# Optimization experiments

Hardware: AMD Instinct MI355X
Metric: run time of the kernel (lower is better)

The kernel has to match this reference:

```python
import jax, jax.numpy as jnp
import numpy as np

jax.config.update("jax_enable_x64", True)  # original torch code runs in float64; minors underflow fp32

D = 96   # Nsites
N = 48   # Nparticles


def setup_inputs() -> dict:
    key = jax.random.key(0)
    # Orthonormal single-particle orbitals (columns), as the module assumes (P^T P = I)
    A = jax.random.normal(key, (D, D), dtype=jnp.float64)
    Q, _ = jnp.linalg.qr(A)
    P = Q[:, :N]  # [D, N]
    # A valid ordered particle configuration: strictly increasing, occ_positions[k] <= D-N+k
    occ_positions = jnp.arange(N, dtype=jnp.int32) * (D // N)  # stride-2 filling
    return {"P": P, "occ_positions": occ_positions}


def _cond_probs(P, occ_positions):
    """Conditional probabilities probs[k, x] of placing the k-th (ordered) particle at
    site x given particles 0..k-1 at occ_positions[0..k-1].

    Math identical to SlaterDetSampler_ordered.get_cond_prob (naive_update=True):
      G = I - P P^T
      probs[k,x] = -det(M_x[0:x+1,0:x+1]) / det(M[0:xmin,0:xmin])
    where M = G - diag(occupancy of particles < k) and M_x additionally sets n_x = 1.
    Since Ksites is always the contiguous range 0..x, all determinants are LEADING
    principal minors; and because only the (x,x) diagonal entry changes by -1 (last index
    of the block), det(M_x block) = d_{x+1} - d_x with d_j the leading j-minor of M.
    """
    Dd, Nn = P.shape
    dt = P.dtype
    eye = jnp.eye(Dd, dtype=dt)
    G = eye - P @ P.T                                             # [D, D]

    onehots = jax.nn.one_hot(occ_positions, Dd, dtype=dt)         # [N, D]
    n_before = jnp.cumsum(onehots, axis=0) - onehots              # occupancy of particles < k
    A = G[None] - n_before[:, :, None] * eye                      # [N, D, D]: G - diag(n_<k)

    # All leading principal minors via batched det of masked matrices:
    # M_j = A on the [0:j,0:j] block, identity elsewhere  =>  det(M_j) = leading j-minor
    ii = jnp.arange(Dd)
    jj = jnp.arange(1, Dd + 1)
    blk = (ii[None, :, None] < jj[:, None, None]) & (ii[None, None, :] < jj[:, None, None])  # [D,D,D]
    Ms = jnp.where(blk[None], A[:, None], eye)                    # [N, D, D, D]
    d = jnp.linalg.det(Ms.reshape(Nn * Dd, Dd, Dd)).reshape(Nn, Dd)
    d_full = jnp.concatenate([jnp.ones((Nn, 1), dt), d], axis=1)  # d_full[k, j] = j-th leading minor

    k = jnp.arange(Nn)
    xmin = jnp.where(k == 0, 0, occ_positions[jnp.maximum(k - 1, 0)] + 1)  # [N]
    xmax = Dd - Nn + k + 1                                                  # [N]
    denom = jnp.take_along_axis(d_full, xmin[:, None], axis=1)              # [N, 1]
    num = d_full[:, 1:] - d_full[:, :-1]                                    # det(GG_num) per candidate x

    x = jnp.arange(Dd)
    support = (x[None, :] >= xmin[:, None]) & (x[None, :] < xmax[:, None])
    probs = jnp.where(support, -num / denom, jnp.zeros((), dt))
    # torch.where(abs(probs) > 1e-15, probs, 0.)
    probs = jnp.where(jnp.abs(probs) > 1e-15, probs, jnp.zeros((), dt))
    return probs


def reference(P, occ_positions):
    probs = _cond_probs(P, occ_positions)                          # [N, D]
    # prob of the full ordered sample = prod_k probs[k, occ_positions[k]]  (as in sample())
    p_k = jnp.take_along_axis(probs, occ_positions[:, None], axis=1)[:, 0]
    prob_sample = jnp.prod(p_k)
    return probs, prob_sample
```

## Files before the change

### kernel.cpp

```cpp
#include <hip/hip_runtime.h>
#include <math.h>

#define Dd 96
#define Nn 48
#define LD 97
#define PTS 98

__device__ __forceinline__ double frcp(double x) {
    double r = __builtin_amdgcn_rcp(x);
    r = fma(fma(-x, r, 1.0), r, r);
    r = fma(fma(-x, r, 1.0), r, r);
    return r;
}

__global__ __launch_bounds__(1024, 1) void slater_kernel(const float* __restrict__ P,
                                                         const int* __restrict__ occ,
                                                         float* __restrict__ out,
                                                         unsigned* __restrict__ cnt) {
    __shared__ double As[Dd * LD];
    __shared__ double fac[2][16];
    __shared__ double ev[2][4];
    __shared__ int    evmask[2];
    __shared__ int    sdead[2];
    __shared__ double gs_runprod;
    __shared__ int    gs_dead;
    __shared__ int    rdy;
    __shared__ unsigned char flag[Dd];
    float* PT = (float*)As;

    const int tid  = threadIdx.x;
    const int k    = blockIdx.x;
    const int n    = Dd - Nn + k + 1;
    const int lane = tid & 63;
    const int wave = tid >> 6;
    const int xmin = (k == 0) ? 0 : occ[k - 1] + 1;

    if (tid == 0) rdy = 0;
    if (tid < Dd) flag[tid] = 0;
    __syncthreads();
    if (tid < k) flag[occ[tid]] = 1;
    for (int e = tid; e < Dd * Nn; e += 1024) {
        int c = e / Nn, t = e - (e / Nn) * Nn;
        PT[t * PTS + c] = P[e];
    }
    __syncthreads();

    double Areg[8]; int trs[2], tcs[2];
#pragma unroll
    for (int it = 0; it < 2; ++it) {
        int tau = tid + 1024 * it;
        double s00 = 0.0, s01 = 0.0, s10 = 0.0, s11 = 0.0;
        int tr = 0, tc = 0;
        if (tau < 1176) {
            tr = (int)((97.0 - sqrt(9409.0 - 8.0 * (double)tau)) * 0.5);
            while ((tr * (97 - tr)) / 2 > tau) --tr;
            while (((tr + 1) * (96 - tr)) / 2 <= tau) ++tr;
            tc = tr + (tau - (tr * (97 - tr)) / 2);
            int r0 = 2 * tr, c0 = 2 * tc;
            if (r0 < n && c0 < n) {
                for (int t = 0; t < Nn; ++t) {
                    const float* row = PT + t * PTS;
                    float2 pr = *(const float2*)(row + r0);
                    float2 pc = *(const float2*)(row + c0);
                    s00 -= (double)pr.x * (double)pc.x; s01 -= (double)pr.x * (double)pc.y;
                    s10 -= (double)pr.y * (double)pc.x; s11 -= (double)pr.y * (double)pc.y;
                }
            }
        }
        trs[it] = tr; tcs[it] = tc;
        Areg[it * 4 + 0] = s00; Areg[it * 4 + 1] = s01;
        Areg[it * 4 + 2] = s10; Areg[it * 4 + 3] = s11;
    }
    __syncthreads();
#pragma unroll
    for (int it = 0; it < 2; ++it) {
        int tau = tid + 1024 * it;
        if (tau < 1176) {
            int tr = trs[it], tc = tcs[it];
            int r0 = 2 * tr, c0 = 2 * tc;
            if (r0 < n && c0 < n) {
                bool r1 = (r0 + 1 < n), c1 = (c0 + 1 < n);
                double d0 = flag[r0] ? 0.0 : 1.0;
                double d1 = flag[r0 + 1] ? 0.0 : 1.0;
                As[r0 * LD + c0] = Areg[it * 4 + 0] + ((r0 == c0) ? d0 : 0.0);
                if (c1)       As[r0 * LD + c0 + 1]       = Areg[it * 4 + 1];
                if (r1)       As[(r0 + 1) * LD + c0]     = Areg[it * 4 + 2];
                if (r1 && c1) As[(r0 + 1) * LD + c0 + 1] = Areg[it * 4 + 3] + ((r0 == c0) ? d1 : 0.0);
                if (tr != tc) {
                    As[c0 * LD + r0] = Areg[it * 4 + 0];
                    if (c1)       As[(c0 + 1) * LD + r0]     = Areg[it * 4 + 1];
                    if (r1)       As[c0 * LD + r0 + 1]       = Areg[it * 4 + 2];
                    if (r1 && c1) As[(c0 + 1) * LD + r0 + 1] = Areg[it * 4 + 3];
                }
            }
        }
    }
    __syncthreads();

    double myprob = 0.0;
    double grun = 1.0;
    int    gdead = 0;

    auto prefactor = [&](int jb, int p) {
        const double* q0 = As + jb * LD + jb;
        const double* q1 = q0 + LD;
        const double* q2 = q1 + LD;
        const double* q3 = q2 + LD;
        double B00=q0[0],B01=q0[1],B02=q0[2],B03=q0[3];
        double B10=q1[0],B11=q1[1],B12=q1[2],B13=q1[3];
        double B20=q2[0],B21=q2[1],B22=q2[2],B23=q2[3];
        double B30=q3[0],B31=q3[1],B32=q3[2],B33=q3[3];
        double piv0=B00, rp0=frcp(piv0);
        double m10=B10*rp0;
        double u01=B01,u02=B02,u03=B03;
        double piv1=B11-m10*u01;
        double u12=B12-m10*u02, u13=B13-m10*u03;
        double rp1=frcp(piv1);
        double m20=B20*rp0;
        double m21=(B21-m20*u01)*rp1;
        double piv2=B22-m20*u02-m21*u12;
        double u23=B23-m20*u03-m21*u13;
        double rp2=frcp(piv2);
        double m30=B30*rp0;
        double m31=(B31-m30*u01)*rp1;
        double m32=(B32-m30*u02-m31*u12)*rp2;
        double piv3=B33-m30*u03-m31*u13-m32*u23;
        double rp3=frcp(piv3);
        double pivs[4]={piv0,piv1,piv2,piv3};
        double evv[4]={0.0,0.0,0.0,0.0};
        int msk=0;
#pragma unroll
        for (int q = 0; q < 4; ++q) {
            if (!gdead) {
                int jj = jb + q;
                double piv = pivs[q];
                double ap = fabs(piv);
                if (jj >= xmin) {
                    evv[q] = grun * (1.0 - piv);
                    msk |= (1 << q);
                    double nr = grun * piv;
                    if (!(ap > 1e-7) || !(ap < 8.0) || !(fabs(nr) > 1e-8)) gdead = 1;
                    else grun = nr;
                } else {
                    if (!(ap > 1e-12) || !(ap < 8.0)) gdead = 1;
                }
            }
        }
        fac[p][0]=m10; fac[p][1]=m20; fac[p][2]=m21; fac[p][3]=m30; fac[p][4]=m31; fac[p][5]=m32;
        fac[p][6]=u01; fac[p][7]=u02; fac[p][8]=u03; fac[p][9]=u12; fac[p][10]=u13; fac[p][11]=u23;
        fac[p][12]=rp0; fac[p][13]=rp1; fac[p][14]=rp2; fac[p][15]=rp3;
        ev[p][0]=evv[0]; ev[p][1]=evv[1]; ev[p][2]=evv[2]; ev[p][3]=evv[3];
        evmask[p]=msk; sdead[p]=gdead;
        gs_runprod=grun; gs_dead=gdead;
    };

    if (wave == 15 && lane == 0) prefactor(0, 0);
    __syncthreads();

    int j = 0, s = 0, target = 4;
    for (; j + 4 <= n - 1; j += 4, ++s) {
        const int par = s & 1;
        if ((tid >> 2) == s) {
            int q = tid & 3;
            if ((evmask[par] >> q) & 1) myprob = ev[par][q];
        }
        if (sdead[par]) break;
        const bool nextex = (j + 8 <= n - 1);

        if (wave == 15) {
            if (nextex) {
                while (__hip_atomic_load(&rdy, __ATOMIC_ACQUIRE,
                                         __HIP_MEMORY_SCOPE_WORKGROUP) < target)
                    __builtin_amdgcn_s_sleep(1);
                target += 4;
                __threadfence_block();
                if (lane == 0) prefactor(j + 4, par ^ 1);
            }
        } else {
            const int t = n - (j + 4);
            const bool ok0 = (lane < t), ok1 = (lane + 64 < t);
            const int c0 = j + 4 + (ok0 ? lane : 0);
            const int c1 = j + 4 + (ok1 ? lane + 64 : 0);
            const double m10=fac[par][0], m20=fac[par][1], m21=fac[par][2],
                         m30=fac[par][3], m31=fac[par][4], m32=fac[par][5];
            const double u01=fac[par][6], u02=fac[par][7], u03=fac[par][8],
                         u12=fac[par][9], u13=fac[par][10], u23=fac[par][11];
            const double rp0=fac[par][12], rp1=fac[par][13],
                         rp2=fac[par][14], rp3=fac[par][15];
            const double R0c0=As[j*LD+c0],     R1c0=As[(j+1)*LD+c0];
            const double R2c0=As[(j+2)*LD+c0], R3c0=As[(j+3)*LD+c0];
            const double R0c1=As[j*LD+c1],     R1c1=As[(j+1)*LD+c1];
            const double R2c1=As[(j+2)*LD+c1], R3c1=As[(j+3)*LD+c1];
            double y0=R0c0, y1=R1c0-m10*y0, y2=R2c0-m20*y0-m21*y1,
                   y3=R3c0-m30*y0-m31*y1-m32*y2;
            double s3c0=y3*rp3, s2c0=(y2-u23*s3c0)*rp2,
                   s1c0=(y1-u12*s2c0-u13*s3c0)*rp1,
                   s0c0=(y0-u01*s1c0-u02*s2c0-u03*s3c0)*rp0;
            double z0=R0c1, z1=R1c1-m10*z0, z2=R2c1-m20*z0-m21*z1,
                   z3=R3c1-m30*z0-m31*z1-m32*z2;
            double s3c1=z3*rp3, s2c1=(z2-u23*s3c1)*rp2,
                   s1c1=(z1-u12*s2c1-u13*s3c1)*rp1,
                   s0c1=(z0-u01*s1c1-u02*s2c1-u03*s3c1)*rp0;

            int i = j + 4 + wave;
            if (i < n) {
                {
                    double* rw = As + i * LD;
                    double a0=rw[j], a1=rw[j+1], a2=rw[j+2], a3=rw[j+3];
                    double T0=rw[c0], T1=rw[c1];
                    double v0=T0 - a0*s0c0 - a1*s1c0 - a2*s2c0 - a3*s3c0;
                    double v1=T1 - a0*s0c1 - a1*s1c1 - a2*s2c1 - a3*s3c1;
                    if (ok0) rw[c0]=v0;
                    if (ok1) rw[c1]=v1;
                }
                if (wave < 4 && nextex) {
                    __threadfence_block();
                    if (lane == 0)
                        __hip_atomic_fetch_add(&rdy, 1, __ATOMIC_RELEASE,
                                               __HIP_MEMORY_SCOPE_WORKGROUP);
                }
                for (i += 15; i < n; i += 15) {
                    double* rw = As + i * LD;
                    double a0=rw[j], a1=rw[j+1], a2=rw[j+2], a3=rw[j+3];
                    double T0=rw[c0], T1=rw[c1];
                    double v0=T0 - a0*s0c0 - a1*s1c0 - a2*s2c0 - a3*s3c0;
                    double v1=T1 - a0*s0c1 - a1*s1c1 - a2*s2c1 - a3*s3c1;
                    if (ok0) rw[c0]=v0;
                    if (ok1) rw[c1]=v1;
                }
            }
        }
        __syncthreads();
    }

    double runprod = gs_runprod;
    bool   dead    = (gs_dead != 0);

    for (; !dead && j < n - 1; ++j) {
        double pivot = As[j * LD + j];
        {
            double ap = fabs(pivot);
            if (j >= xmin) {
                if (tid == j) myprob = runprod * (1.0 - pivot);
                double nr = runprod * pivot;
                if (!(ap > 1e-7) || !(ap < 8.0) || !(fabs(nr) > 1e-8)) dead = true;
                else runprod = nr;
            } else {
                if (!(ap > 1e-12) || !(ap < 8.0)) dead = true;
            }
        }
        if (dead) break;
        double rp = frcp(pivot);
        int t = n - 1 - j;
        double r0 = (lane < t)      ? As[j * LD + j + 1 + lane]  : 0.0;
        double r1 = (lane + 64 < t) ? As[j * LD + j + 65 + lane] : 0.0;
        for (int i = j + 1 + wave; i < n; i += 16) {
            double mult = As[i * LD + j] * rp;
            if (lane < t)      As[i * LD + j + 1 + lane]  -= mult * r0;
            if (lane + 64 < t) As[i * LD + j + 65 + lane] -= mult * r1;
        }
        __syncthreads();
    }
    if (!dead && tid == n - 1) {
        double pl = As[(n - 1) * LD + (n - 1)];
        myprob = runprod * (1.0 - pl);
    }

    if (tid < Dd) {
        double p = myprob;
        if (!isfinite(p)) p = 0.0;
        if (!(fabs(p) > 1e-15)) p = 0.0;
        p = fmin(fmax(p, 0.0), 1.0);
        out[k * Dd + tid] = (float)p;
    }

    __threadfence();
    __syncthreads();
    if (wave == 0) {
        int old = 0;
        if (lane == 0)
            old = (int)__hip_atomic_fetch_add(cnt, 1u, __ATOMIC_ACQ_REL,
                                              __HIP_MEMORY_SCOPE_AGENT);
        old = __shfl(old, 0, 64);
        if (((unsigned)old + 1u) % (unsigned)Nn == 0u) {
            __threadfence();
            double v = 1.0;
            if (lane < Nn) {
                float f = __hip_atomic_load(out + lane * Dd + occ[lane],
                                            __ATOMIC_RELAXED, __HIP_MEMORY_SCOPE_AGENT);
                v = (double)f;
            }
#pragma unroll
            for (int off = 32; off >= 1; off >>= 1)
                v *= __shfl_down(v, off, 64);
            if (lane == 0) {
                if (!isfinite(v)) v = 0.0;
                out[Nn * Dd] = (float)v;
            }
        }
    }
}

extern "C" void kernel_launch(void* const* d_in, const int* in_sizes, int n_in,
                              void* d_out, int out_size, void* d_ws, size_t ws_size,
                              hipStream_t stream) {
    const float* P = (const float*)d_in[0];
    const int* occ = (const int*)d_in[1];
    float* out = (float*)d_out;

    slater_kernel<<<Nn, 1024, 0, stream>>>(P, occ, out, (unsigned*)d_ws);
}
```

Baseline: 105.8 us.

## Keep matrix rows in registers with 6-wide block LU per wave

Replaces the shared-memory 4-column blocked LU, which used a dedicated factor wave and an atomic ready counter, with a register-resident scheme. Each wave owns 6 rows held in registers. At each step one wave factors the 6x6 diagonal block via shuffles, solves for the multipliers and publishes them through shared Sbuf/aBuf buffers. All remaining waves then apply a rank-6 update from registers. This removes the LDS read-modify-write traffic and the spin-wait synchronisation, at the cost of more registers, a serial factor step on the critical path between barriers, and fewer but wider steps.

```diff
diff --git a/kernel.cpp b/kernel.cpp
--- a/kernel.cpp
+++ b/kernel.cpp
@@ -18,13 +18,12 @@
                                                          float* __restrict__ out,
                                                          unsigned* __restrict__ cnt) {
     __shared__ double As[Dd * LD];
-    __shared__ double fac[2][16];
-    __shared__ double ev[2][4];
-    __shared__ int    evmask[2];
-    __shared__ int    sdead[2];
+    __shared__ double Sbuf[2][6][Dd];
+    __shared__ double aBuf[2][Dd][6];
+    __shared__ double ev[2][6];
+    __shared__ int    evmask[2], sdead[2];
     __shared__ double gs_runprod;
     __shared__ int    gs_dead;
-    __shared__ int    rdy;
     __shared__ unsigned char flag[Dd];
     float* PT = (float*)As;
 
@@ -35,7 +34,6 @@
     const int wave = tid >> 6;
     const int xmin = (k == 0) ? 0 : occ[k - 1] + 1;
 
-    if (tid == 0) rdy = 0;
     if (tid < Dd) flag[tid] = 0;
     __syncthreads();
     if (tid < k) flag[occ[tid]] = 1;
@@ -98,140 +96,149 @@
     __syncthreads();
 
     double myprob = 0.0;
-    double grun = 1.0;
-    int    gdead = 0;
-
-    auto prefactor = [&](int jb, int p) {
-        const double* q0 = As + jb * LD + jb;
-        const double* q1 = q0 + LD;
-        const double* q2 = q1 + LD;
-        const double* q3 = q2 + LD;
-        double B00=q0[0],B01=q0[1],B02=q0[2],B03=q0[3];
-        double B10=q1[0],B11=q1[1],B12=q1[2],B13=q1[3];
-        double B20=q2[0],B21=q2[1],B22=q2[2],B23=q2[3];
-        double B30=q3[0],B31=q3[1],B32=q3[2],B33=q3[3];
-        double piv0=B00, rp0=frcp(piv0);
-        double m10=B10*rp0;
-        double u01=B01,u02=B02,u03=B03;
-        double piv1=B11-m10*u01;
-        double u12=B12-m10*u02, u13=B13-m10*u03;
-        double rp1=frcp(piv1);
-        double m20=B20*rp0;
-        double m21=(B21-m20*u01)*rp1;
-        double piv2=B22-m20*u02-m21*u12;
-        double u23=B23-m20*u03-m21*u13;
-        double rp2=frcp(piv2);
-        double m30=B30*rp0;
-        double m31=(B31-m30*u01)*rp1;
-        double m32=(B32-m30*u02-m31*u12)*rp2;
-        double piv3=B33-m30*u03-m31*u13-m32*u23;
-        double rp3=frcp(piv3);
-        double pivs[4]={piv0,piv1,piv2,piv3};
-        double evv[4]={0.0,0.0,0.0,0.0};
-        int msk=0;
-#pragma unroll
-        for (int q = 0; q < 4; ++q) {
-            if (!gdead) {
-                int jj = jb + q;
-                double piv = pivs[q];
-                double ap = fabs(piv);
-                if (jj >= xmin) {
-                    evv[q] = grun * (1.0 - piv);
-                    msk |= (1 << q);
-                    double nr = grun * piv;
-                    if (!(ap > 1e-7) || !(ap < 8.0) || !(fabs(nr) > 1e-8)) gdead = 1;
-                    else grun = nr;
-                } else {
-                    if (!(ap > 1e-12) || !(ap < 8.0)) gdead = 1;
-                }
-            }
-        }
-        fac[p][0]=m10; fac[p][1]=m20; fac[p][2]=m21; fac[p][3]=m30; fac[p][4]=m31; fac[p][5]=m32;
-        fac[p][6]=u01; fac[p][7]=u02; fac[p][8]=u03; fac[p][9]=u12; fac[p][10]=u13; fac[p][11]=u23;
-        fac[p][12]=rp0; fac[p][13]=rp1; fac[p][14]=rp2; fac[p][15]=rp3;
-        ev[p][0]=evv[0]; ev[p][1]=evv[1]; ev[p][2]=evv[2]; ev[p][3]=evv[3];
-        evmask[p]=msk; sdead[p]=gdead;
-        gs_runprod=grun; gs_dead=gdead;
+    double rr[6][2];
+
+    auto prefactor = [&](int jb, int p, double grun, int gdead) {
+        double Bd[6][6], rp[6];
+#pragma unroll
+        for (int u = 0; u < 6; ++u) {
+#pragma unroll
+            for (int r = 0; r < 6; ++r)
+                Bd[u][r] = __shfl((r & 1) ? rr[u][1] : rr[u][0], (jb + r) >> 1, 64);
+        }
+#pragma unroll
+        for (int cc = 0; cc < 6; ++cc) {
+            rp[cc] = frcp(Bd[cc][cc]);
+#pragma unroll
+            for (int i = cc + 1; i < 6; ++i) {
+                double m = Bd[i][cc] * rp[cc];
+                Bd[i][cc] = m;
+#pragma unroll
+                for (int r = cc + 1; r < 6; ++r) Bd[i][r] -= m * Bd[cc][r];
+            }
+        }
+        if (lane == 0) {
+            int msk = 0; double evv[6];
+#pragma unroll
+            for (int q = 0; q < 6; ++q) {
+                evv[q] = 0.0;
+                if (!gdead) {
+                    int jj = jb + q;
+                    double pv = Bd[q][q];
+                    double ap = fabs(pv);
+                    if (jj >= xmin) {
+                        evv[q] = grun * (1.0 - pv);
+                        msk |= (1 << q);
+                        double nr = grun * pv;
+                        if (!(ap > 1e-7) || !(ap < 8.0) || !(fabs(nr) > 1e-8)) gdead = 1;
+                        else grun = nr;
+                    } else {
+                        if (!(ap > 1e-12) || !(ap < 8.0)) gdead = 1;
+                    }
+                }
+            }
+#pragma unroll
+            for (int q = 0; q < 6; ++q) ev[p][q] = evv[q];
+            evmask[p] = msk; sdead[p] = gdead;
+            gs_runprod = grun; gs_dead = gdead;
+        }
+        if (lane < 48) {
+            const bool live = (2 * lane >= jb + 6);
+#pragma unroll
+            for (int sl = 0; sl < 2; ++sl) {
+                double y0 = rr[0][sl];
+                double y1 = rr[1][sl] - Bd[1][0] * y0;
+                double y2 = rr[2][sl] - Bd[2][0] * y0 - Bd[2][1] * y1;
+                double y3 = rr[3][sl] - Bd[3][0] * y0 - Bd[3][1] * y1 - Bd[3][2] * y2;
+                double y4 = rr[4][sl] - Bd[4][0] * y0 - Bd[4][1] * y1 - Bd[4][2] * y2 - Bd[4][3] * y3;
+                double y5 = rr[5][sl] - Bd[5][0] * y0 - Bd[5][1] * y1 - Bd[5][2] * y2 - Bd[5][3] * y3 - Bd[5][4] * y4;
+                double s5 = y5 * rp[5];
+                double s4 = (y4 - Bd[4][5] * s5) * rp[4];
+                double s3 = (y3 - Bd[3][4] * s4 - Bd[3][5] * s5) * rp[3];
+                double s2 = (y2 - Bd[2][3] * s3 - Bd[2][4] * s4 - Bd[2][5] * s5) * rp[2];
+                double s1 = (y1 - Bd[1][2] * s2 - Bd[1][3] * s3 - Bd[1][4] * s4 - Bd[1][5] * s5) * rp[1];
+                double s0 = (y0 - Bd[0][1] * s1 - Bd[0][2] * s2 - Bd[0][3] * s3 - Bd[0][4] * s4 - Bd[0][5] * s5) * rp[0];
+                Sbuf[p][0][2 * lane + sl] = live ? s0 : 0.0;
+                Sbuf[p][1][2 * lane + sl] = live ? s1 : 0.0;
+                Sbuf[p][2][2 * lane + sl] = live ? s2 : 0.0;
+                Sbuf[p][3][2 * lane + sl] = live ? s3 : 0.0;
+                Sbuf[p][4][2 * lane + sl] = live ? s4 : 0.0;
+                Sbuf[p][5][2 * lane + sl] = live ? s5 : 0.0;
+            }
+        }
     };
 
-    if (wave == 15 && lane == 0) prefactor(0, 0);
-    __syncthreads();
-
-    int j = 0, s = 0, target = 4;
-    for (; j + 4 <= n - 1; j += 4, ++s) {
+#pragma unroll
+    for (int u = 0; u < 6; ++u) {
+        if (lane < 48) {
+            rr[u][0] = As[(6 * wave + u) * LD + 2 * lane];
+            rr[u][1] = As[(6 * wave + u) * LD + 2 * lane + 1];
+        } else { rr[u][0] = 0.0; rr[u][1] = 0.0; }
+    }
+    if (wave >= 1 && lane < 3) {
+#pragma unroll
+        for (int u = 0; u < 6; ++u) {
+            aBuf[0][6 * wave + u][2 * lane]     = rr[u][0];
+            aBuf[0][6 * wave + u][2 * lane + 1] = rr[u][1];
+        }
+    }
+    if (wave == 0) prefactor(0, 0, 1.0, 0);
+    __syncthreads();
+
+    int j = 0, s = 0;
+    for (; j + 6 <= n - 1; j += 6, ++s) {
         const int par = s & 1;
-        if ((tid >> 2) == s) {
-            int q = tid & 3;
+        if (tid >= j && tid < j + 6) {
+            int q = tid - j;
             if ((evmask[par] >> q) & 1) myprob = ev[par][q];
         }
         if (sdead[par]) break;
-        const bool nextex = (j + 8 <= n - 1);
-
-        if (wave == 15) {
-            if (nextex) {
-                while (__hip_atomic_load(&rdy, __ATOMIC_ACQUIRE,
-                                         __HIP_MEMORY_SCOPE_WORKGROUP) < target)
-                    __builtin_amdgcn_s_sleep(1);
-                target += 4;
-                __threadfence_block();
-                if (lane == 0) prefactor(j + 4, par ^ 1);
-            }
-        } else {
-            const int t = n - (j + 4);
-            const bool ok0 = (lane < t), ok1 = (lane + 64 < t);
-            const int c0 = j + 4 + (ok0 ? lane : 0);
-            const int c1 = j + 4 + (ok1 ? lane + 64 : 0);
-            const double m10=fac[par][0], m20=fac[par][1], m21=fac[par][2],
-                         m30=fac[par][3], m31=fac[par][4], m32=fac[par][5];
-            const double u01=fac[par][6], u02=fac[par][7], u03=fac[par][8],
-                         u12=fac[par][9], u13=fac[par][10], u23=fac[par][11];
-            const double rp0=fac[par][12], rp1=fac[par][13],
-                         rp2=fac[par][14], rp3=fac[par][15];
-            const double R0c0=As[j*LD+c0],     R1c0=As[(j+1)*LD+c0];
-            const double R2c0=As[(j+2)*LD+c0], R3c0=As[(j+3)*LD+c0];
-            const double R0c1=As[j*LD+c1],     R1c1=As[(j+1)*LD+c1];
-            const double R2c1=As[(j+2)*LD+c1], R3c1=As[(j+3)*LD+c1];
-            double y0=R0c0, y1=R1c0-m10*y0, y2=R2c0-m20*y0-m21*y1,
-                   y3=R3c0-m30*y0-m31*y1-m32*y2;
-            double s3c0=y3*rp3, s2c0=(y2-u23*s3c0)*rp2,
-                   s1c0=(y1-u12*s2c0-u13*s3c0)*rp1,
-                   s0c0=(y0-u01*s1c0-u02*s2c0-u03*s3c0)*rp0;
-            double z0=R0c1, z1=R1c1-m10*z0, z2=R2c1-m20*z0-m21*z1,
-                   z3=R3c1-m30*z0-m31*z1-m32*z2;
-            double s3c1=z3*rp3, s2c1=(z2-u23*s3c1)*rp2,
-                   s1c1=(z1-u12*s2c1-u13*s3c1)*rp1,
-                   s0c1=(z0-u01*s1c1-u02*s2c1-u03*s3c1)*rp0;
-
-            int i = j + 4 + wave;
-            if (i < n) {
-                {
-                    double* rw = As + i * LD;
-                    double a0=rw[j], a1=rw[j+1], a2=rw[j+2], a3=rw[j+3];
-                    double T0=rw[c0], T1=rw[c1];
-                    double v0=T0 - a0*s0c0 - a1*s1c0 - a2*s2c0 - a3*s3c0;
-                    double v1=T1 - a0*s0c1 - a1*s1c1 - a2*s2c1 - a3*s3c1;
-                    if (ok0) rw[c0]=v0;
-                    if (ok1) rw[c1]=v1;
-                }
-                if (wave < 4 && nextex) {
-                    __threadfence_block();
-                    if (lane == 0)
-                        __hip_atomic_fetch_add(&rdy, 1, __ATOMIC_RELEASE,
-                                               __HIP_MEMORY_SCOPE_WORKGROUP);
-                }
-                for (i += 15; i < n; i += 15) {
-                    double* rw = As + i * LD;
-                    double a0=rw[j], a1=rw[j+1], a2=rw[j+2], a3=rw[j+3];
-                    double T0=rw[c0], T1=rw[c1];
-                    double v0=T0 - a0*s0c0 - a1*s1c0 - a2*s2c0 - a3*s3c0;
-                    double v1=T1 - a0*s0c1 - a1*s1c1 - a2*s2c1 - a3*s3c1;
-                    if (ok0) rw[c0]=v0;
-                    if (ok1) rw[c1]=v1;
-                }
-            }
+        const bool nexts = (j + 12 <= n - 1);
+
+        if (wave >= s + 1) {
+            if (lane < 48) {
+                double S0[6], S1[6];
+#pragma unroll
+                for (int r = 0; r < 6; ++r) {
+                    double2 sv = *(const double2*)&Sbuf[par][r][2 * lane];
+                    S0[r] = sv.x; S1[r] = sv.y;
+                }
+#pragma unroll
+                for (int u = 0; u < 6; ++u) {
+                    const double* ab = &aBuf[par][6 * wave + u][0];
+                    double2 q0 = *(const double2*)(ab + 0);
+                    double2 q1 = *(const double2*)(ab + 2);
+                    double2 q2 = *(const double2*)(ab + 4);
+                    rr[u][0] -= q0.x * S0[0] + q0.y * S0[1] + q1.x * S0[2]
+                              + q1.y * S0[3] + q2.x * S0[4] + q2.y * S0[5];
+                    rr[u][1] -= q0.x * S1[0] + q0.y * S1[1] + q1.x * S1[2]
+                              + q1.y * S1[3] + q2.x * S1[4] + q2.y * S1[5];
+                }
+                if (nexts && wave >= s + 2) {
+                    int d = lane - 3 * (s + 1);
+                    if (d >= 0 && d < 3) {
+#pragma unroll
+                        for (int u = 0; u < 6; ++u) {
+                            aBuf[par ^ 1][6 * wave + u][2 * d]     = rr[u][0];
+                            aBuf[par ^ 1][6 * wave + u][2 * d + 1] = rr[u][1];
+                        }
+                    }
+                }
+            }
+            if (nexts && wave == s + 1)
+                prefactor(j + 6, par ^ 1, gs_runprod, gs_dead);
         }
         __syncthreads();
     }
+
+    if (lane < 48) {
+#pragma unroll
+        for (int u = 0; u < 6; ++u) {
+            As[(6 * wave + u) * LD + 2 * lane]     = rr[u][0];
+            As[(6 * wave + u) * LD + 2 * lane + 1] = rr[u][1];
+        }
+    }
+    __syncthreads();
 
     double runprod = gs_runprod;
     bool   dead    = (gs_dead != 0);
```

After: 100.9 us. -4.7%, faster.
